# Kernel optimization log

Measured on AMD Instinct MI355X. Metric: run time of the kernel, lower is better.

## Reference

```python
import jax, jax.numpy as jnp
import numpy as np

N = 100000   # nodes
E = 3200000  # edges
G = 64       # graphs
L = 4        # conv layers
D = 64       # conv channel
BN_EPS = 1e-5


def setup_inputs() -> dict:
    key = jax.random.key(0)
    ks = jax.random.split(key, 16)
    s = 0.05
    inp = {
        "x": jax.random.normal(ks[0], (N, D), jnp.float32),
        "edge_index": jax.random.randint(ks[1], (2, E), 0, N, jnp.int32),
        "batch": jnp.sort(jax.random.randint(ks[2], (N,), 0, G, jnp.int32)),
        "conv_W": jax.random.normal(ks[3], (L, D, D), jnp.float32) * s,
        "conv_b": jax.random.normal(ks[4], (L, D), jnp.float32) * s,
        "bn_gamma": jax.random.uniform(ks[5], (L, D), jnp.float32) + 0.5,
        "bn_beta": jax.random.normal(ks[6], (L, D), jnp.float32) * s,
        "bn_mean": jnp.zeros((L, D), jnp.float32),
        "bn_var": jnp.ones((L, D), jnp.float32),
        "enc_W1": jax.random.normal(ks[7], (L * D, 256), jnp.float32) * s,
        "enc_b1": jax.random.normal(ks[8], (256,), jnp.float32) * s,
        "enc_W2": jax.random.normal(ks[9], (256, 128), jnp.float32) * s,
        "enc_b2": jax.random.normal(ks[10], (128,), jnp.float32) * s,
        "dec_W1": jax.random.normal(ks[11], (128, 64), jnp.float32) * s,
        "dec_b1": jax.random.normal(ks[12], (64,), jnp.float32) * s,
        "dec_W2": jax.random.normal(ks[13], (64, 1), jnp.float32) * s,
        "dec_b2": jax.random.normal(ks[14], (1,), jnp.float32) * s,
    }
    return inp


def reference(x, edge_index, batch, conv_W, conv_b, bn_gamma, bn_beta, bn_mean,
              bn_var, enc_W1, enc_b1, enc_W2, enc_b2, dec_W1, dec_b1, dec_W2, dec_b2):
    n = x.shape[0]
    # GCN normalization (self-loops + symmetric deg^-1/2), computed once.
    loops = jnp.arange(n, dtype=edge_index.dtype)
    row = jnp.concatenate([edge_index[0], loops])  # source
    col = jnp.concatenate([edge_index[1], loops])  # target
    deg = jax.ops.segment_sum(jnp.ones_like(col, jnp.float32), col, num_segments=n)
    dis = jax.lax.rsqrt(deg)  # deg >= 1 due to self-loops
    norm = (dis[row] * dis[col])[:, None]  # [E+N, 1]

    num_layers = conv_W.shape[0]
    skip = 2  # num_skip_layers
    previous_outputs = []
    for i in range(num_layers):
        xw = x @ conv_W[i]                                       # [N, D]
        msg = xw[row] * norm                                     # gather + scale
        x = jax.ops.segment_sum(msg, col, num_segments=n) + conv_b[i]
        # BatchNorm1d (eval: running stats)
        x = (x - bn_mean[i]) * (bn_gamma[i] * jax.lax.rsqrt(bn_var[i] + BN_EPS)) + bn_beta[i]
        x = jax.nn.relu(x)
        if i % skip == 0 and i != 0 and i != num_layers - 1:
            x = x + previous_outputs[i - skip]
        previous_outputs.append(x)

    local = jnp.concatenate(previous_outputs, axis=1)            # [N, L*D]
    h = jax.nn.relu(local @ enc_W1 + enc_b1)
    h = jax.nn.relu(h @ enc_W2 + enc_b2)                         # [N, 128]

    # scatter_mean over graphs
    sums = jax.ops.segment_sum(h, batch, num_segments=G)
    cnt = jax.ops.segment_sum(jnp.ones((n,), h.dtype), batch, num_segments=G)
    gfeat = sums / jnp.maximum(cnt, 1.0)[:, None]                # [G, 128]

    out = jax.nn.relu(gfeat @ dec_W1 + dec_b1)
    out = out @ dec_W2 + dec_b2                                  # [G, 1]
    return jnp.squeeze(out, 1)                                   # num_classes == 1
```

## Files before the change

kernel.cpp:

```cpp
#include <hip/hip_runtime.h>
#include <cstdint>
#include <cstddef>

#define D 64
#define SMAX 24
#define PCHUNK 8192
#define BCAP 12288

typedef __attribute__((ext_vector_type(8))) short short8;
typedef __attribute__((ext_vector_type(4))) float floatx4;
typedef __attribute__((ext_vector_type(2))) float floatx2;
typedef __attribute__((ext_vector_type(8))) _Float16 half8v;

__device__ inline unsigned short f2bf(float f) {
    unsigned u = __float_as_uint(f);
    unsigned r = 0x7FFFu + ((u >> 16) & 1u);
    return (unsigned short)((u + r) >> 16);
}
__device__ inline float bf2f(unsigned short h) {
    return __uint_as_float(((unsigned)h) << 16);
}
__device__ inline unsigned char f2fp8(float f) {
    int pk = __builtin_amdgcn_cvt_pk_fp8_f32(f, f, 0, false);
    return (unsigned char)(pk & 0xFF);
}


__global__ void k_hist(const int* __restrict__ col, int* __restrict__ ghist,
                       int E, int NBK) {
    extern __shared__ int lh[];
    int t = threadIdx.x;
    for (int i = t; i < NBK; i += 256) lh[i] = 0;
    __syncthreads();
    int base = blockIdx.x * 8192;
    int end = base + 8192; if (end > E) end = E;
    for (int e = base + t; e < end; e += 256) atomicAdd(&lh[col[e] >> 8], 1);
    __syncthreads();
    for (int i = t; i < NBK; i += 256) if (lh[i]) atomicAdd(&ghist[i], lh[i]);
}

__global__ void k_bscan(const int* __restrict__ ghist, int* __restrict__ bstart,
                        int* __restrict__ gcur, int* __restrict__ offs,
                        int NBK, int N, int E) {
    __shared__ int s[512];
    int t = threadIdx.x;
    int v = (t < NBK) ? ghist[t] : 0;
    s[t] = v; __syncthreads();
    for (int off = 1; off < 512; off <<= 1) {
        int x = (t >= off) ? s[t - off] : 0;
        __syncthreads();
        s[t] += x;
        __syncthreads();
    }
    int excl = s[t] - v;
    if (t < NBK) { bstart[t] = excl; gcur[t] = excl; }
    if (t == 0) { bstart[NBK] = E; offs[N] = E; }
}

__global__ __launch_bounds__(512) void k_part(const int* __restrict__ row,
                                              const int* __restrict__ col,
                                              int* __restrict__ gcur,
                                              unsigned* __restrict__ part,
                                              int E, int NBK) {
    extern __shared__ int sm[];
    int* cnt    = sm;
    int* cursor = sm + NBK;
    int* delta  = sm + 2 * NBK;
    int* s      = sm + 3 * NBK;
    unsigned* sbuf = (unsigned*)(sm + 3 * NBK + 512);
    unsigned short* bkt = (unsigned short*)(sbuf + PCHUNK);

    int t = threadIdx.x;
    int base = blockIdx.x * PCHUNK;
    int end = base + PCHUNK; if (end > E) end = E;
    int nloc = end - base;

    for (int i = t; i < NBK; i += 512) cnt[i] = 0;
    __syncthreads();

    int carr[16];
#pragma unroll
    for (int i = 0; i < 16; ++i) {
        int e = base + t + i * 512;
        int c = -1;
        if (e < end) {
            c = col[e];
            atomicAdd(&cnt[c >> 8], 1);
        }
        carr[i] = c;
    }
    __syncthreads();

    int v0 = (t < NBK) ? cnt[t] : 0;
    s[t] = v0;
    __syncthreads();
    for (int off = 1; off < 512; off <<= 1) {
        int x = (t >= off) ? s[t - off] : 0;
        __syncthreads();
        s[t] += x;
        __syncthreads();
    }
    for (int i = t; i < NBK; i += 512) {
        int c = cnt[i];
        int lst = s[i] - c;
        cursor[i] = lst;
        int gb = c ? atomicAdd(&gcur[i], c) : 0;
        delta[i] = gb - lst;
    }
    __syncthreads();

#pragma unroll
    for (int i = 0; i < 16; ++i) {
        int c = carr[i];
        if (c >= 0) {
            int e = base + t + i * 512;
            int b = c >> 8;
            int p = atomicAdd(&cursor[b], 1);
            sbuf[p] = ((unsigned)row[e] << 8) | (unsigned)(c & 255);
            bkt[p] = (unsigned short)b;
        }
    }
    __syncthreads();

    for (int p = t; p < nloc; p += 512) {
        int b = bkt[p];
        part[p + delta[b]] = sbuf[p];
    }
}

__global__ __launch_bounds__(256) void k_bucket(const unsigned* __restrict__ part,
                                                const int* __restrict__ bstart,
                                                int* __restrict__ offs,
                                                float* __restrict__ dis,
                                                int* __restrict__ csrc, int N) {
    __shared__ int ncnt[256];
    __shared__ int s[256];
    __shared__ int lcur[256];
    __shared__ unsigned sb[BCAP];
    int b = blockIdx.x;
    int t = threadIdx.x;
    int n0 = b << 8;
    int e0 = bstart[b], e1 = bstart[b + 1];
    int nloc = e1 - e0;
    bool fits = nloc <= BCAP;
    ncnt[t] = 0;
    __syncthreads();
    if (fits) {
        for (int e = t; e < nloc; e += 256) {
            unsigned pr = part[e0 + e];
            sb[e] = pr;
            atomicAdd(&ncnt[pr & 255u], 1);
        }
    } else {
        for (int e = e0 + t; e < e1; e += 256) {
            unsigned pr = part[e];
            atomicAdd(&ncnt[pr & 255u], 1);
        }
    }
    __syncthreads();
    int v = ncnt[t];
    s[t] = v; __syncthreads();
    for (int off = 1; off < 256; off <<= 1) {
        int x = (t >= off) ? s[t - off] : 0;
        __syncthreads();
        s[t] += x;
        __syncthreads();
    }
    int excl = s[t] - v;
    int node = n0 + t;
    if (node < N) {
        offs[node] = e0 + excl;
        dis[node] = rsqrtf((float)(v + 1));
    }
    lcur[t] = excl;
    __syncthreads();
    if (fits) {
        for (int e = t; e < nloc; e += 256) {
            unsigned pr = sb[e];
            int p = atomicAdd(&lcur[pr & 255u], 1);
            csrc[e0 + p] = (int)(pr >> 8) << 6;
        }
    } else {
        for (int e = e0 + t; e < e1; e += 256) {
            unsigned pr = part[e];
            int p = atomicAdd(&lcur[pr & 255u], 1);
            csrc[e0 + p] = (int)(pr >> 8) << 6;
        }
    }
}

__global__ void k_gb(const int* __restrict__ batch, int* __restrict__ gstart,
                     int N, int G) {
    int g = threadIdx.x;
    if (g > G) return;
    int lo = 0, hi = N;
    while (lo < hi) {
        int mid = (lo + hi) >> 1;
        if (batch[mid] < g) lo = mid + 1; else hi = mid;
    }
    gstart[g] = lo;
}

__global__ void k_bnprep(const float* __restrict__ cb, const float* __restrict__ g,
                         const float* __restrict__ be, const float* __restrict__ mu,
                         const float* __restrict__ var, float* __restrict__ sc,
                         float* __restrict__ sh, int LD) {
    int i = blockIdx.x * 256 + threadIdx.x;
    if (i < LD) {
        float s = g[i] * rsqrtf(var[i] + 1e-5f);
        sc[i] = s;
        sh[i] = (cb[i] - mu[i]) * s + be[i];
    }
}

__global__ void k_wpack(const float* __restrict__ B, unsigned short* __restrict__ hiP,
                        unsigned short* __restrict__ loP, int K, int Nc, int nshift) {
    int idx = blockIdx.x * 256 + threadIdx.x;
    if (idx >= K * Nc) return;
    int k = idx >> nshift;
    int n = idx & (Nc - 1);
    float a = B[idx];
    unsigned b = __float_as_uint(a);
    unsigned hb = b & 0xFFFF0000u;
    float ah = __uint_as_float(hb);
    float al = a - ah;
    int c = k >> 5;
    int ntile = n >> 6;
    int j = (n & 63) >> 4;
    int lane = ((k & 31) >> 3) * 16 + (n & 15);
    int kidx = k & 7;
    size_t o = ((((size_t)c * (Nc >> 6) + ntile) * 4 + j) * 64 + lane) * 8 + kidx;
    hiP[o] = (unsigned short)(hb >> 16);
    loP[o] = (unsigned short)(__float_as_uint(al) >> 16);
}

__global__ void k_wpackb(const float* __restrict__ B, unsigned short* __restrict__ P,
                         int K, int Nc, int nshift) {
    int idx = blockIdx.x * 256 + threadIdx.x;
    if (idx >= K * Nc) return;
    int k = idx >> nshift;
    int n = idx & (Nc - 1);
    int c = k >> 5;
    int ntile = n >> 6;
    int j = (n & 63) >> 4;
    int lane = ((k & 31) >> 3) * 16 + (n & 15);
    int kidx = k & 7;
    size_t o = ((((size_t)c * (Nc >> 6) + ntile) * 4 + j) * 64 + lane) * 8 + kidx;
    P[o] = f2bf(B[idx]);
}

__global__ void k_cast(const float* __restrict__ x, unsigned short* __restrict__ xb,
                       int n8) {
    int i = blockIdx.x * 256 + threadIdx.x;
    if (i >= n8) return;
    const float4* p = (const float4*)(x + (size_t)i * 8);
    float4 v0 = p[0], v1 = p[1];
    short8 o;
    o[0] = (short)f2bf(v0.x); o[1] = (short)f2bf(v0.y);
    o[2] = (short)f2bf(v0.z); o[3] = (short)f2bf(v0.w);
    o[4] = (short)f2bf(v1.x); o[5] = (short)f2bf(v1.y);
    o[6] = (short)f2bf(v1.z); o[7] = (short)f2bf(v1.w);
    *(short8*)(xb + (size_t)i * 8) = o;
}


__global__ __launch_bounds__(256) void k_convm(const unsigned short* __restrict__ A,
                                               const unsigned short* __restrict__ Whi,
                                               const unsigned short* __restrict__ Wlo,
                                               const float* __restrict__ dis,
                                               unsigned char* __restrict__ out, int N) {
    int t = threadIdx.x;
    int lane = t & 63;
    int l16 = lane & 15;
    int quad = lane >> 4;
    int w = t >> 6;
    int bm = blockIdx.x * 128 + w * 32;

    floatx4 acc[2][4];
#pragma unroll
    for (int i = 0; i < 2; ++i)
#pragma unroll
        for (int j = 0; j < 4; ++j) acc[i][j] = (floatx4)0.f;

    int r0 = bm + l16; if (r0 > N - 1) r0 = N - 1;
    int r1 = bm + 16 + l16; if (r1 > N - 1) r1 = N - 1;
    const unsigned short* a0 = A + (size_t)r0 * 64 + quad * 8;
    const unsigned short* a1 = A + (size_t)r1 * 64 + quad * 8;
    const unsigned short* bp = Whi + lane * 8;
    size_t loOff = (size_t)(Wlo - Whi);

    short8 a0c[2], a1c[2], bh[2][4], bl[2][4];
#pragma unroll
    for (int c = 0; c < 2; ++c) {
        a0c[c] = *(const short8*)(a0 + c * 32);
        a1c[c] = *(const short8*)(a1 + c * 32);
#pragma unroll
        for (int j = 0; j < 4; ++j) {
            bh[c][j] = *(const short8*)(bp + c * 2048 + j * 512);
            bl[c][j] = *(const short8*)(bp + loOff + c * 2048 + j * 512);
        }
    }
#pragma unroll
    for (int c = 0; c < 2; ++c) {
#pragma unroll
        for (int j = 0; j < 4; ++j) {
            acc[0][j] = __builtin_amdgcn_mfma_f32_16x16x32_bf16(a0c[c], bl[c][j], acc[0][j], 0, 0, 0);
            acc[0][j] = __builtin_amdgcn_mfma_f32_16x16x32_bf16(a0c[c], bh[c][j], acc[0][j], 0, 0, 0);
            acc[1][j] = __builtin_amdgcn_mfma_f32_16x16x32_bf16(a1c[c], bl[c][j], acc[1][j], 0, 0, 0);
            acc[1][j] = __builtin_amdgcn_mfma_f32_16x16x32_bf16(a1c[c], bh[c][j], acc[1][j], 0, 0, 0);
        }
    }
#pragma unroll
    for (int i = 0; i < 2; ++i) {
#pragma unroll
        for (int r = 0; r < 4; ++r) {
            int m = bm + i * 16 + quad * 4 + r;
            if (m < N) {
                float dv = dis[m];
                unsigned char* op = out + (size_t)m * 64 + l16;
#pragma unroll
                for (int j = 0; j < 4; ++j)
                    op[j * 16] = f2fp8(acc[i][j][r] * dv);
            }
        }
    }
}


__global__ __launch_bounds__(256) void k_agg(const unsigned char* __restrict__ xw,
                                             const int* __restrict__ offs,
                                             const int* __restrict__ src,
                                             const float* __restrict__ dis,
                                             const float* __restrict__ sc,
                                             const float* __restrict__ sh,
                                             const float* __restrict__ skip,
                                             float* __restrict__ out,
                                             unsigned short* __restrict__ outb,
                                             int N) {
    int t = threadIdx.x;
    int lane = t & 63;
    int w = t >> 6;
    int g = lane >> 3;
    int cg = lane & 7;
    int c0 = cg * 8;
    int v = blockIdx.x * 32 + w * 8 + g;
    int vc = (v < N) ? v : N - 1;
    int e0 = offs[vc], e1 = offs[vc + 1];
    int deg = (v < N) ? (e1 - e0) : 0;
    const int* sp = src + e0;
    const unsigned char* xb = xw + (cg << 3);
    int zoff = N << 6;

    int dm = deg;
    dm = max(dm, __shfl_xor(dm, 8));
    dm = max(dm, __shfl_xor(dm, 16));
    dm = max(dm, __shfl_xor(dm, 32));

    floatx2 a01 = (floatx2)0.f, a23 = (floatx2)0.f;
    floatx2 a45 = (floatx2)0.f, a67 = (floatx2)0.f;

    int gbase = g << 3;
    for (int k = 0; k < dm; k += 8) {
        int idx = k + cg;
        int sv = sp[(idx < deg) ? idx : 0];
        uint2 m[8];
#pragma unroll
        for (int j = 0; j < 8; ++j) {
            int o = __shfl(sv, gbase + j);
            o = (k + j < deg) ? o : zoff;
            m[j] = *(const uint2*)(xb + o);
        }
#pragma unroll
        for (int j = 0; j < 8; ++j) {
            a01 += __builtin_amdgcn_cvt_pk_f32_fp8(m[j].x, false);
            a23 += __builtin_amdgcn_cvt_pk_f32_fp8(m[j].x, true);
            a45 += __builtin_amdgcn_cvt_pk_f32_fp8(m[j].y, false);
            a67 += __builtin_amdgcn_cvt_pk_f32_fp8(m[j].y, true);
        }
    }

    if (v < N) {
        uint2 ar = *(const uint2*)(xb + ((size_t)vc << 6));
        a01 += __builtin_amdgcn_cvt_pk_f32_fp8(ar.x, false);
        a23 += __builtin_amdgcn_cvt_pk_f32_fp8(ar.x, true);
        a45 += __builtin_amdgcn_cvt_pk_f32_fp8(ar.y, false);
        a67 += __builtin_amdgcn_cvt_pk_f32_fp8(ar.y, true);
        float u[8];
        u[0] = a01[0]; u[1] = a01[1]; u[2] = a23[0]; u[3] = a23[1];
        u[4] = a45[0]; u[5] = a45[1]; u[6] = a67[0]; u[7] = a67[1];
        float dv = dis[vc];
        float4 S0 = *(const float4*)&sc[c0];
        float4 S1 = *(const float4*)&sc[c0 + 4];
        float4 H0 = *(const float4*)&sh[c0];
        float4 H1 = *(const float4*)&sh[c0 + 4];
        float sv[8], hv[8];
        sv[0] = S0.x; sv[1] = S0.y; sv[2] = S0.z; sv[3] = S0.w;
        sv[4] = S1.x; sv[5] = S1.y; sv[6] = S1.z; sv[7] = S1.w;
        hv[0] = H0.x; hv[1] = H0.y; hv[2] = H0.z; hv[3] = H0.w;
        hv[4] = H1.x; hv[5] = H1.y; hv[6] = H1.z; hv[7] = H1.w;
        float y[8];
#pragma unroll
        for (int q = 0; q < 8; ++q)
            y[q] = fmaxf(fmaf(u[q] * dv, sv[q], hv[q]), 0.f);
        size_t ob = (size_t)v * 64 + c0;
        if (skip) {
            float4 k0v = *(const float4*)(skip + ob);
            float4 k1v = *(const float4*)(skip + ob + 4);
            y[0] += k0v.x; y[1] += k0v.y; y[2] += k0v.z; y[3] += k0v.w;
            y[4] += k1v.x; y[5] += k1v.y; y[6] += k1v.z; y[7] += k1v.w;
        }
        if (out) {
            float4 o0, o1;
            o0.x = y[0]; o0.y = y[1]; o0.z = y[2]; o0.w = y[3];
            o1.x = y[4]; o1.y = y[5]; o1.z = y[6]; o1.w = y[7];
            *(float4*)(out + ob) = o0;
            *(float4*)(out + ob + 4) = o1;
        }
        short8 b8;
#pragma unroll
        for (int q = 0; q < 8; ++q) b8[q] = (short)f2bf(y[q]);
        *(short8*)(outb + ob) = b8;
    }
}


__global__ __launch_bounds__(256) void k_encb(const unsigned short* __restrict__ A,
                                              size_t pplane, int rowstr,
                                              int M, int K, int WN,
                                              const unsigned short* __restrict__ BP,
                                              const float* __restrict__ bias,
                                              unsigned short* __restrict__ Cb,
                                              float* __restrict__ Cf, int ldc) {
    extern __shared__ unsigned short As[];
    int t = threadIdx.x;
    int lane = t & 63;
    int l16 = lane & 15;
    int quad = lane >> 4;
    int w = t >> 6;
    int nw = w % WN;
    int mg = w / WN;
    int BM = 32 * (4 / WN);
    int blockM0 = blockIdx.x * BM;
    int n0 = nw * 64;
    int NC = K >> 5;
    int KP = K + 8;
    size_t cstr = (size_t)(ldc >> 6) * 2048;

    int segPerRow = K >> 3;
    int sshift = 31 - __clz(segPerRow);
    int totalSeg = BM << sshift;
    for (int q = t; q < totalSeg; q += 256) {
        int r = q >> sshift;
        int s = q - (r << sshift);
        int gr = blockM0 + r; if (gr > M - 1) gr = M - 1;
        int p = s >> 3;
        int i = s & 7;
        *(short8*)(As + r * KP + s * 8) =
            *(const short8*)(A + (size_t)p * pplane + (size_t)gr * rowstr + i * 8);
    }
    __syncthreads();

    floatx4 acc[2][4];
#pragma unroll
    for (int i = 0; i < 2; ++i)
#pragma unroll
        for (int j = 0; j < 4; ++j) acc[i][j] = (floatx4)0.f;

    const unsigned short* a0 = As + (mg * 32 + l16) * KP + quad * 8;
    const unsigned short* a1 = a0 + 16 * KP;
    const unsigned short* bp = BP + ((size_t)(n0 >> 6) * 4) * 512 + lane * 8;

    short8 B[2][4];
#pragma unroll
    for (int s = 0; s < 2; ++s) {
        int cc = (s < NC) ? s : NC - 1;
#pragma unroll
        for (int j = 0; j < 4; ++j)
            B[s][j] = *(const short8*)(bp + (size_t)cc * cstr + j * 512);
    }

    for (int c = 0; c < NC; ++c) {
        int nc = (c + 2 < NC) ? c + 2 : NC - 1;
        short8 tB[4];
#pragma unroll
        for (int j = 0; j < 4; ++j)
            tB[j] = *(const short8*)(bp + (size_t)nc * cstr + j * 512);
        short8 A0 = *(const short8*)(a0 + c * 32);
        short8 A1 = *(const short8*)(a1 + c * 32);
#pragma unroll
        for (int j = 0; j < 4; ++j) {
            acc[0][j] = __builtin_amdgcn_mfma_f32_16x16x32_bf16(A0, B[0][j], acc[0][j], 0, 0, 0);
            acc[1][j] = __builtin_amdgcn_mfma_f32_16x16x32_bf16(A1, B[0][j], acc[1][j], 0, 0, 0);
        }
#pragma unroll
        for (int j = 0; j < 4; ++j) B[0][j] = B[1][j];
#pragma unroll
        for (int j = 0; j < 4; ++j) B[1][j] = tB[j];
    }

    int bm = blockM0 + mg * 32;
#pragma unroll
    for (int i = 0; i < 2; ++i) {
#pragma unroll
        for (int r = 0; r < 4; ++r) {
            int m = bm + i * 16 + quad * 4 + r;
            if (m < M) {
#pragma unroll
                for (int j = 0; j < 4; ++j) {
                    float y = fmaxf(acc[i][j][r] + bias[n0 + j * 16 + l16], 0.f);
                    size_t idx = (size_t)m * ldc + n0 + j * 16 + l16;
                    if (Cb) Cb[idx] = f2bf(y);
                    else    Cf[idx] = y;
                }
            }
        }
    }
}


__global__ __launch_bounds__(256) void k_pool(const float* __restrict__ h2,
                                              const int* __restrict__ gstart,
                                              float* __restrict__ gsum, int H) {
    int g = blockIdx.x / SMAX;
    int s = blockIdx.x % SMAX;
    int base = gstart[g], end = gstart[g + 1];
    int cnt = end - base;
    if (cnt <= 0) return;
    int per = (cnt + SMAX - 1) / SMAX;
    int n0 = base + s * per;
    int n1 = n0 + per; if (n1 > end) n1 = end;
    if (n0 >= n1) return;
    int t = threadIdx.x;
    int q = t & 31;
    int c = q * 4;
    int sub = t >> 5;
    float4 acc = make_float4(0.f, 0.f, 0.f, 0.f);
    for (int n = n0 + sub; n < n1; n += 8) {
        float4 v = *(const float4*)(h2 + (size_t)n * H + c);
        acc.x += v.x; acc.y += v.y; acc.z += v.z; acc.w += v.w;
    }
    __shared__ float4 red[8][32];
    red[sub][q] = acc;
    __syncthreads();
    if (sub == 0) {
        float4 a = red[0][q];
#pragma unroll
        for (int i = 1; i < 8; ++i) {
            float4 b = red[i][q];
            a.x += b.x; a.y += b.y; a.z += b.z; a.w += b.w;
        }
        atomicAdd(&gsum[(size_t)g * H + c + 0], a.x);
        atomicAdd(&gsum[(size_t)g * H + c + 1], a.y);
        atomicAdd(&gsum[(size_t)g * H + c + 2], a.z);
        atomicAdd(&gsum[(size_t)g * H + c + 3], a.w);
    }
}


__global__ __launch_bounds__(256) void k_dec(const float* __restrict__ gsum, const int* __restrict__ gstart,
                      const float* __restrict__ W1, const float* __restrict__ b1,
                      const float* __restrict__ W2, const float* __restrict__ b2,
                      float* __restrict__ out, int H, int HD) {
    __shared__ float red[4][64];
    int g = blockIdx.x;
    int t = threadIdx.x;
    int c = t & 63;
    int kk = t >> 6;
    float cnt = (float)(gstart[g + 1] - gstart[g]);
    float inv = 1.0f / fmaxf(cnt, 1.0f);
    const float* gp = gsum + (size_t)g * 128 + kk * 32;
    const float* wp = W1 + (size_t)(kk * 32) * 64 + c;
    float a0 = 0.f, a1 = 0.f, a2 = 0.f, a3 = 0.f;
#pragma unroll
    for (int j = 0; j < 32; j += 4) {
        float g0 = gp[j + 0], g1 = gp[j + 1], g2 = gp[j + 2], g3 = gp[j + 3];
        float w0 = wp[(j + 0) * 64], w1 = wp[(j + 1) * 64];
        float w2 = wp[(j + 2) * 64], w3 = wp[(j + 3) * 64];
        a0 = fmaf(g0, w0, a0);
        a1 = fmaf(g1, w1, a1);
        a2 = fmaf(g2, w2, a2);
        a3 = fmaf(g3, w3, a3);
    }
    red[kk][c] = (a0 + a1) + (a2 + a3);
    __syncthreads();
    if (kk == 0) {
        float hid = ((red[0][c] + red[1][c]) + (red[2][c] + red[3][c])) * inv + b1[c];
        hid = fmaxf(hid, 0.f);
        float p = hid * W2[c];
        for (int off = 32; off > 0; off >>= 1) p += __shfl_down(p, off);
        if (c == 0) out[g] = p + b2[0];
    }
}


extern "C" void kernel_launch(void* const* d_in, const int* in_sizes, int n_in,
                              void* d_out, int out_size, void* d_ws, size_t ws_size,
                              hipStream_t stream) {
    const float* x     = (const float*)d_in[0];
    const int*   ei    = (const int*)d_in[1];
    const int*   batch = (const int*)d_in[2];
    const float* convW = (const float*)d_in[3];
    const float* convb = (const float*)d_in[4];
    const float* gamma = (const float*)d_in[5];
    const float* beta  = (const float*)d_in[6];
    const float* mean  = (const float*)d_in[7];
    const float* var   = (const float*)d_in[8];
    const float* eW1   = (const float*)d_in[9];
    const float* eb1   = (const float*)d_in[10];
    const float* eW2   = (const float*)d_in[11];
    const float* eb2   = (const float*)d_in[12];
    const float* dW1   = (const float*)d_in[13];
    const float* db1   = (const float*)d_in[14];
    const float* dW2   = (const float*)d_in[15];
    const float* db2   = (const float*)d_in[16];

    int N  = in_sizes[0] / D;
    int E  = in_sizes[1] / 2;
    int L  = in_sizes[3] / (D * D);
    int G  = out_size;
    int LD = L * D;
    int H1 = in_sizes[10];
    int H2 = in_sizes[12];
    int HD = in_sizes[14];
    int NBK = (N + 255) >> 8;

    char* ws = (char*)d_ws;
    size_t off = 0;
    auto alloc = [&](size_t b) -> void* {
        void* p = ws + off;
        off += (b + 255) & ~(size_t)255;
        return p;
    };
    float* local  = (float*)alloc((size_t)N * H2 * 4);
    unsigned short* localb = (unsigned short*)alloc((size_t)N * LD * 2);
    char*  bufB   = (char*)alloc((size_t)(N + 1) * LD * 2);
    unsigned short* xb = (unsigned short*)alloc((size_t)N * D * 2);
    int*   csrc   = (int*)alloc((size_t)E * 4);
    float* dis    = (float*)alloc((size_t)N * 4);
    int*   offs   = (int*)alloc((size_t)(N + 1) * 4);
    int*   ghist  = (int*)alloc((size_t)NBK * 4);
    int*   bstart = (int*)alloc((size_t)(NBK + 1) * 4);
    int*   gcur   = (int*)alloc((size_t)NBK * 4);
    float* sc     = (float*)alloc((size_t)LD * 4);
    float* sh     = (float*)alloc((size_t)LD * 4);
    float* gsum   = (float*)alloc((size_t)G * H2 * 4);
    int*   gstart = (int*)alloc((size_t)(G + 1) * 4);
    unsigned short* w1p  = (unsigned short*)alloc((size_t)LD * H1 * 2);
    unsigned short* w2p  = (unsigned short*)alloc((size_t)H1 * H2 * 2);
    unsigned short* wchi = (unsigned short*)alloc((size_t)L * D * D * 2);
    unsigned short* wclo = (unsigned short*)alloc((size_t)L * D * D * 2);
    unsigned* part = (unsigned*)bufB;
    unsigned char* xw = (unsigned char*)bufB;
    unsigned short* h1b = (unsigned short*)bufB;
    float* h2 = local;

    hipMemsetAsync(ghist, 0, (size_t)NBK * 4, stream);
    hipMemsetAsync(gsum, 0, (size_t)G * H2 * 4, stream);

    int nchunks = (E + PCHUNK - 1) / PCHUNK;
    k_hist<<<nchunks, 256, NBK * 4, stream>>>(ei + E, ghist, E, NBK);
    k_bscan<<<1, 512, 0, stream>>>(ghist, bstart, gcur, offs, NBK, N, E);
    int partLds = (3 * NBK + 512) * 4 + PCHUNK * 4 + PCHUNK * 2;
    k_part<<<nchunks, 512, partLds, stream>>>(ei, ei + E, gcur, part, E, NBK);
    k_bucket<<<NBK, 256, 0, stream>>>(part, bstart, offs, dis, csrc, N);
    hipMemsetAsync(xw + (size_t)N * 64, 0, 64, stream);
    k_gb<<<1, 128, 0, stream>>>(batch, gstart, N, G);
    k_bnprep<<<(LD + 255) / 256, 256, 0, stream>>>(convb, gamma, beta, mean, var, sc, sh, LD);
    k_wpackb<<<(LD * H1 + 255) / 256, 256, 0, stream>>>(eW1, w1p, LD, H1, 8);
    k_wpackb<<<(H1 * H2 + 255) / 256, 256, 0, stream>>>(eW2, w2p, H1, H2, 7);
    for (int l = 0; l < L; ++l)
        k_wpack<<<(D * D + 255) / 256, 256, 0, stream>>>(convW + (size_t)l * D * D,
                                                         wchi + (size_t)l * D * D,
                                                         wclo + (size_t)l * D * D, D, D, 6);
    k_cast<<<(N * D / 8 + 255) / 256, 256, 0, stream>>>(x, xb, N * D / 8);

    size_t plane = (size_t)N * 64;
    for (int l = 0; l < L; ++l) {
        const unsigned short* Ain = (l == 0) ? xb : (localb + (size_t)(l - 1) * plane);
        k_convm<<<(N + 127) / 128, 256, 0, stream>>>(Ain,
                                                     wchi + (size_t)l * D * D,
                                                     wclo + (size_t)l * D * D,
                                                     dis, xw, N);
        const float* skip = (l % 2 == 0 && l != 0 && l != L - 1) ? local : nullptr;
        float* outf = (l == 0) ? local : nullptr;
        k_agg<<<(N + 31) / 32, 256, 0, stream>>>(xw, offs, csrc, dis, sc + (size_t)l * D,
                                                 sh + (size_t)l * D, skip,
                                                 outf,
                                                 localb + (size_t)l * plane, N);
    }

    int lds1 = 32 * (LD + 8) * 2;
    k_encb<<<(N + 31) / 32, 256, lds1, stream>>>(localb, plane, 64, N, LD, 4, w1p, eb1,
                                                 h1b, nullptr, H1);
    int lds2 = 64 * (H1 + 8) * 2;
    k_encb<<<(N + 63) / 64, 256, lds2, stream>>>(h1b, 64, H1, N, H1, 2, w2p, eb2,
                                                 nullptr, h2, H2);

    k_pool<<<G * SMAX, 256, 0, stream>>>(h2, gstart, gsum, H2);
    k_dec<<<G, 256, 0, stream>>>(gsum, gstart, dW1, db1, dW2, db2, (float*)d_out, H2, HD);
}
```

Measured before the change: 503.6 us.

## Fuse both encoder GEMMs and graph mean-pool into one kernel

```diff
diff --git a/kernel.cpp b/kernel.cpp
--- a/kernel.cpp
+++ b/kernel.cpp
@@ -424,67 +424,68 @@
 }
 
 
-__global__ __launch_bounds__(256) void k_encb(const unsigned short* __restrict__ A,
-                                              size_t pplane, int rowstr,
-                                              int M, int K, int WN,
-                                              const unsigned short* __restrict__ BP,
-                                              const float* __restrict__ bias,
-                                              unsigned short* __restrict__ Cb,
-                                              float* __restrict__ Cf, int ldc) {
-    extern __shared__ unsigned short As[];
+__global__ __launch_bounds__(256) void k_enc(const unsigned short* __restrict__ A,
+                                             size_t pplane, int M,
+                                             const unsigned short* __restrict__ BP1,
+                                             const float* __restrict__ bias1,
+                                             const unsigned short* __restrict__ BP2,
+                                             const float* __restrict__ bias2,
+                                             const int* __restrict__ batch,
+                                             float* __restrict__ gsum) {
+    __shared__ unsigned short As[32 * 264];
+    __shared__ int bt[32];
+    __shared__ int badf;
+    const int KP = 264;
     int t = threadIdx.x;
     int lane = t & 63;
     int l16 = lane & 15;
     int quad = lane >> 4;
     int w = t >> 6;
-    int nw = w % WN;
-    int mg = w / WN;
-    int BM = 32 * (4 / WN);
-    int blockM0 = blockIdx.x * BM;
-    int n0 = nw * 64;
-    int NC = K >> 5;
-    int KP = K + 8;
-    size_t cstr = (size_t)(ldc >> 6) * 2048;
-
-    int segPerRow = K >> 3;
-    int sshift = 31 - __clz(segPerRow);
-    int totalSeg = BM << sshift;
-    for (int q = t; q < totalSeg; q += 256) {
-        int r = q >> sshift;
-        int s = q - (r << sshift);
-        int gr = blockM0 + r; if (gr > M - 1) gr = M - 1;
+    int bm = blockIdx.x * 32;
+
+    if (t == 0) badf = 0;
+    if (t < 32) bt[t] = batch[min(bm + t, M - 1)];
+
+    for (int q = t; q < 1024; q += 256) {
+        int r = q >> 5;
+        int s = q & 31;
+        int gr = bm + r; if (gr > M - 1) gr = M - 1;
         int p = s >> 3;
         int i = s & 7;
         *(short8*)(As + r * KP + s * 8) =
-            *(const short8*)(A + (size_t)p * pplane + (size_t)gr * rowstr + i * 8);
-    }
-    __syncthreads();
-
+            *(const short8*)(A + (size_t)p * pplane + (size_t)gr * 64 + i * 8);
+    }
+    __syncthreads();
+
+    if (t < 32) {
+        int b = bt[t];
+        if (b != bt[0] && b != bt[31]) badf = 1;
+    }
+
+    int n0 = w * 64;
     floatx4 acc[2][4];
 #pragma unroll
     for (int i = 0; i < 2; ++i)
 #pragma unroll
         for (int j = 0; j < 4; ++j) acc[i][j] = (floatx4)0.f;
 
-    const unsigned short* a0 = As + (mg * 32 + l16) * KP + quad * 8;
+    const unsigned short* a0 = As + l16 * KP + quad * 8;
     const unsigned short* a1 = a0 + 16 * KP;
-    const unsigned short* bp = BP + ((size_t)(n0 >> 6) * 4) * 512 + lane * 8;
+    const unsigned short* bp1 = BP1 + ((size_t)(n0 >> 6) * 4) * 512 + lane * 8;
 
     short8 B[2][4];
 #pragma unroll
-    for (int s = 0; s < 2; ++s) {
-        int cc = (s < NC) ? s : NC - 1;
+    for (int s = 0; s < 2; ++s)
 #pragma unroll
         for (int j = 0; j < 4; ++j)
-            B[s][j] = *(const short8*)(bp + (size_t)cc * cstr + j * 512);
-    }
-
-    for (int c = 0; c < NC; ++c) {
-        int nc = (c + 2 < NC) ? c + 2 : NC - 1;
+            B[s][j] = *(const short8*)(bp1 + (size_t)s * 8192 + j * 512);
+
+    for (int c = 0; c < 8; ++c) {
+        int nc = (c + 2 < 8) ? c + 2 : 7;
         short8 tB[4];
 #pragma unroll
         for (int j = 0; j < 4; ++j)
-            tB[j] = *(const short8*)(bp + (size_t)nc * cstr + j * 512);
+            tB[j] = *(const short8*)(bp1 + (size_t)nc * 8192 + j * 512);
         short8 A0 = *(const short8*)(a0 + c * 32);
         short8 A1 = *(const short8*)(a1 + c * 32);
 #pragma unroll
@@ -498,61 +499,80 @@
         for (int j = 0; j < 4; ++j) B[1][j] = tB[j];
     }
 
-    int bm = blockM0 + mg * 32;
-#pragma unroll
-    for (int i = 0; i < 2; ++i) {
+    __syncthreads();
+
+#pragma unroll
+    for (int i = 0; i < 2; ++i)
 #pragma unroll
         for (int r = 0; r < 4; ++r) {
-            int m = bm + i * 16 + quad * 4 + r;
-            if (m < M) {
-#pragma unroll
-                for (int j = 0; j < 4; ++j) {
-                    float y = fmaxf(acc[i][j][r] + bias[n0 + j * 16 + l16], 0.f);
-                    size_t idx = (size_t)m * ldc + n0 + j * 16 + l16;
-                    if (Cb) Cb[idx] = f2bf(y);
-                    else    Cf[idx] = y;
+            int ml = i * 16 + quad * 4 + r;
+#pragma unroll
+            for (int j = 0; j < 4; ++j) {
+                float y = fmaxf(acc[i][j][r] + bias1[n0 + j * 16 + l16], 0.f);
+                As[ml * KP + n0 + j * 16 + l16] = f2bf(y);
+            }
+        }
+    __syncthreads();
+
+    int n0b = w * 32;
+    floatx4 acc2[2][2];
+#pragma unroll
+    for (int i = 0; i < 2; ++i)
+#pragma unroll
+        for (int j = 0; j < 2; ++j) acc2[i][j] = (floatx4)0.f;
+
+    const unsigned short* bp2 = BP2 +
+        ((size_t)((n0b >> 6) * 4 + ((n0b & 63) >> 4))) * 512 + lane * 8;
+
+    for (int c = 0; c < 8; ++c) {
+        short8 A0 = *(const short8*)(a0 + c * 32);
+        short8 A1 = *(const short8*)(a1 + c * 32);
+        short8 B0 = *(const short8*)(bp2 + (size_t)c * 4096);
+        short8 B1 = *(const short8*)(bp2 + (size_t)c * 4096 + 512);
+        acc2[0][0] = __builtin_amdgcn_mfma_f32_16x16x32_bf16(A0, B0, acc2[0][0], 0, 0, 0);
+        acc2[0][1] = __builtin_amdgcn_mfma_f32_16x16x32_bf16(A0, B1, acc2[0][1], 0, 0, 0);
+        acc2[1][0] = __builtin_amdgcn_mfma_f32_16x16x32_bf16(A1, B0, acc2[1][0], 0, 0, 0);
+        acc2[1][1] = __builtin_amdgcn_mfma_f32_16x16x32_bf16(A1, B1, acc2[1][1], 0, 0, 0);
+    }
+
+    int g0 = bt[0], g1 = bt[31];
+    if (!badf) {
+#pragma unroll
+        for (int j = 0; j < 2; ++j) {
+            float s0 = 0.f, s1 = 0.f;
+#pragma unroll
+            for (int i = 0; i < 2; ++i)
+#pragma unroll
+                for (int r = 0; r < 4; ++r) {
+                    int ml = i * 16 + quad * 4 + r;
+                    if (bm + ml < M) {
+                        float y = fmaxf(acc2[i][j][r] + bias2[n0b + j * 16 + l16], 0.f);
+                        bool f = (bt[ml] != g0);
+                        s0 += f ? 0.f : y;
+                        s1 += f ? y : 0.f;
+                    }
                 }
+            s0 += __shfl_xor(s0, 16); s0 += __shfl_xor(s0, 32);
+            s1 += __shfl_xor(s1, 16); s1 += __shfl_xor(s1, 32);
+            if (quad == 0) {
+                int cb = n0b + j * 16 + l16;
+                atomicAdd(&gsum[(size_t)g0 * 128 + cb], s0);
+                if (g1 != g0) atomicAdd(&gsum[(size_t)g1 * 128 + cb], s1);
             }
         }
-    }
-}
-
-
-__global__ __launch_bounds__(256) void k_pool(const float* __restrict__ h2,
-                                              const int* __restrict__ gstart,
-                                              float* __restrict__ gsum, int H) {
-    int g = blockIdx.x / SMAX;
-    int s = blockIdx.x % SMAX;
-    int base = gstart[g], end = gstart[g + 1];
-    int cnt = end - base;
-    if (cnt <= 0) return;
-    int per = (cnt + SMAX - 1) / SMAX;
-    int n0 = base + s * per;
-    int n1 = n0 + per; if (n1 > end) n1 = end;
-    if (n0 >= n1) return;
-    int t = threadIdx.x;
-    int q = t & 31;
-    int c = q * 4;
-    int sub = t >> 5;
-    float4 acc = make_float4(0.f, 0.f, 0.f, 0.f);
-    for (int n = n0 + sub; n < n1; n += 8) {
-        float4 v = *(const float4*)(h2 + (size_t)n * H + c);
-        acc.x += v.x; acc.y += v.y; acc.z += v.z; acc.w += v.w;
-    }
-    __shared__ float4 red[8][32];
-    red[sub][q] = acc;
-    __syncthreads();
-    if (sub == 0) {
-        float4 a = red[0][q];
-#pragma unroll
-        for (int i = 1; i < 8; ++i) {
-            float4 b = red[i][q];
-            a.x += b.x; a.y += b.y; a.z += b.z; a.w += b.w;
-        }
-        atomicAdd(&gsum[(size_t)g * H + c + 0], a.x);
-        atomicAdd(&gsum[(size_t)g * H + c + 1], a.y);
-        atomicAdd(&gsum[(size_t)g * H + c + 2], a.z);
-        atomicAdd(&gsum[(size_t)g * H + c + 3], a.w);
+    } else {
+#pragma unroll
+        for (int j = 0; j < 2; ++j)
+#pragma unroll
+            for (int i = 0; i < 2; ++i)
+#pragma unroll
+                for (int r = 0; r < 4; ++r) {
+                    int ml = i * 16 + quad * 4 + r;
+                    if (bm + ml < M) {
+                        float y = fmaxf(acc2[i][j][r] + bias2[n0b + j * 16 + l16], 0.f);
+                        atomicAdd(&gsum[(size_t)bt[ml] * 128 + n0b + j * 16 + l16], y);
+                    }
+                }
     }
 }
 
@@ -631,7 +651,7 @@
         off += (b + 255) & ~(size_t)255;
         return p;
     };
-    float* local  = (float*)alloc((size_t)N * H2 * 4);
+    float* local  = (float*)alloc((size_t)N * D * 4);
     unsigned short* localb = (unsigned short*)alloc((size_t)N * LD * 2);
     char*  bufB   = (char*)alloc((size_t)(N + 1) * LD * 2);
     unsigned short* xb = (unsigned short*)alloc((size_t)N * D * 2);
@@ -651,8 +671,6 @@
     unsigned short* wclo = (unsigned short*)alloc((size_t)L * D * D * 2);
     unsigned* part = (unsigned*)bufB;
     unsigned char* xw = (unsigned char*)bufB;
-    unsigned short* h1b = (unsigned short*)bufB;
-    float* h2 = local;
 
     hipMemsetAsync(ghist, 0, (size_t)NBK * 4, stream);
     hipMemsetAsync(gsum, 0, (size_t)G * H2 * 4, stream);
@@ -689,13 +707,8 @@
                                                  localb + (size_t)l * plane, N);
     }
 
-    int lds1 = 32 * (LD + 8) * 2;
-    k_encb<<<(N + 31) / 32, 256, lds1, stream>>>(localb, plane, 64, N, LD, 4, w1p, eb1,
-                                                 h1b, nullptr, H1);
-    int lds2 = 64 * (H1 + 8) * 2;
-    k_encb<<<(N + 63) / 64, 256, lds2, stream>>>(h1b, 64, H1, N, H1, 2, w2p, eb2,
-                                                 nullptr, h2, H2);
-
-    k_pool<<<G * SMAX, 256, 0, stream>>>(h2, gstart, gsum, H2);
+    k_enc<<<(N + 31) / 32, 256, 0, stream>>>(localb, plane, N, w1p, eb1, w2p, eb2,
+                                             batch, gsum);
+
     k_dec<<<G, 256, 0, stream>>>(gsum, gstart, dW1, db1, dW2, db2, (float*)d_out, H2, HD);
 }
```

After: 458.0 us. 1.1x faster.
